# Kernel optimization log

Measured on AMD Instinct MI355X. Metric: run time of the kernel, lower is better.

Reference implementation:

```python
import jax, jax.numpy as jnp
import numpy as np

MARGIN = 0.3
EPS = 1e-12

def setup_inputs() -> dict:
    key = jax.random.key(0)
    k1, k2 = jax.random.split(key)
    n, d, num_classes = 8192, 512, 512
    inputs = jax.random.normal(k1, (n, d), dtype=jnp.float32)
    targets = jax.random.randint(k2, (n,), 0, num_classes, dtype=jnp.int64)
    return {"inputs": inputs, "targets": targets}

def reference(inputs, targets):
    n = inputs.shape[0]
    # pairwise Euclidean distances: ||xi||^2 + ||xj||^2 - 2 xi.xj, clamped & sqrt'd
    sq = jnp.sum(inputs * inputs, axis=1)  # [n]
    dist2 = sq[:, None] + sq[None, :] - 2.0 * (inputs @ inputs.T)
    dist = jnp.sqrt(jnp.clip(dist2, EPS, None))  # [n, n]
    mask = targets[:, None] == targets[None, :]  # [n, n] same-identity mask
    neg_inf = jnp.asarray(-jnp.inf, dist.dtype)
    pos_inf = jnp.asarray(jnp.inf, dist.dtype)
    dist_ap = jnp.max(jnp.where(mask, dist, neg_inf), axis=1)   # hardest positive per row
    dist_an = jnp.min(jnp.where(mask, pos_inf, dist), axis=1)   # hardest negative per row
    # MarginRankingLoss with y=1, mean reduction: mean(relu(dist_ap - dist_an + margin))
    loss = jnp.mean(jnp.maximum(dist_ap - dist_an + MARGIN, 0.0))
    return loss
```

## Files before the change

### kernel.cpp

```cpp
#include <hip/hip_runtime.h>

#define N 8192
#define D 512
#define NSB 32
#define NFULL 1024
#define NQ 64
#define NBRICKS (NFULL + NQ)
#define MARGIN 0.3f

typedef __attribute__((ext_vector_type(4))) int int4v;
typedef __attribute__((ext_vector_type(8))) int int8v;
typedef __attribute__((ext_vector_type(4))) float f32x4;

__device__ __forceinline__ void gload_lds16(const void* g, void* l) {
    __builtin_amdgcn_global_load_lds(
        (const __attribute__((address_space(1))) void*)g,
        (__attribute__((address_space(3))) void*)l,
        16, 0, 0);
}

__device__ __forceinline__ int8v load_frag8(const unsigned char* base, int row, int q) {
    const int v = (2 * q) ^ (row & 7);
    int4v lo = *(const int4v*)(base + row * 128 + v * 16);
    int4v hi = *(const int4v*)(base + row * 128 + (v ^ 1) * 16);
    return __builtin_shufflevector(lo, hi, 0, 1, 2, 3, 4, 5, 6, 7);
}

__global__ void prep_kernel(const float* __restrict__ x,
                            unsigned char* __restrict__ x8,
                            float* __restrict__ sq,
                            unsigned int* __restrict__ apU,
                            unsigned int* __restrict__ anU,
                            int* __restrict__ cnt) {
    if (blockIdx.x == 0 && threadIdx.x == 0) cnt[0] = 0;
    int w = threadIdx.x >> 6, lane = threadIdx.x & 63;
    int row = blockIdx.x * 4 + w;
    const float4* p = (const float4*)(x + (size_t)row * D) + lane * 2;
    float4 v0 = p[0], v1 = p[1];
    float s = v0.x * v0.x + v0.y * v0.y + v0.z * v0.z + v0.w * v0.w
            + v1.x * v1.x + v1.y * v1.y + v1.z * v1.z + v1.w * v1.w;
    int w0 = __builtin_amdgcn_cvt_pk_fp8_f32(v0.x, v0.y, 0, false);
    w0     = __builtin_amdgcn_cvt_pk_fp8_f32(v0.z, v0.w, w0, true);
    int w1 = __builtin_amdgcn_cvt_pk_fp8_f32(v1.x, v1.y, 0, false);
    w1     = __builtin_amdgcn_cvt_pk_fp8_f32(v1.z, v1.w, w1, true);
    ((int2*)(x8 + (size_t)row * D))[lane] = make_int2(w0, w1);
    #pragma unroll
    for (int o = 32; o > 0; o >>= 1) s += __shfl_xor(s, o);
    if (lane == 0) {
        sq[row] = s;
        apU[row] = 0u;
        anU[row] = 0x7f800000u;
    }
}

template <int TN>
__device__ __forceinline__ void brick_body(
    int rowBase, int colBase,
    const unsigned char* __restrict__ xb, const float* __restrict__ sq,
    const int* __restrict__ tgt,
    unsigned int* __restrict__ apU, unsigned int* __restrict__ anU,
    char* smem_raw, float* sqI, float* sqJ, int* tI, int* tJ) {
    constexpr int NC = TN * 32;
    unsigned char* Asm = (unsigned char*)smem_raw;
    unsigned char* Bsm = Asm + 128 * 128;
    float* redAp = (float*)smem_raw;
    float* redAn = redAp + 128 * 34;
    float* colAp = (float*)smem_raw;
    float* colAn = colAp + NC * 10;

    const int tid = threadIdx.x;
    const int w = tid >> 6, lane = tid & 63, q = lane >> 4, c = lane & 15;
    const int wm = w & 1, wn = w >> 1;

    if (tid < 128) { sqI[tid] = sq[rowBase + tid]; tI[tid] = tgt[rowBase + tid]; }
    if (tid < NC)  { sqJ[tid] = sq[colBase + tid]; tJ[tid] = tgt[colBase + tid]; }

    const unsigned char* Ag = xb + (size_t)rowBase * D;
    const unsigned char* Bg = xb + (size_t)colBase * D;

    f32x4 acc[4][TN] = {};

    for (int k0 = 0; k0 < D; k0 += 128) {
        #pragma unroll
        for (int s = 0; s < 4; s++) {
            int p = s * 256 + tid;
            int r = p >> 3, kc = (p & 7) ^ (r & 7);
            gload_lds16(Ag + (size_t)r * D + k0 + kc * 16, Asm + p * 16);
        }
        #pragma unroll
        for (int s = 0; s < TN; s++) {
            int p = s * 256 + tid;
            int r = p >> 3, kc = (p & 7) ^ (r & 7);
            gload_lds16(Bg + (size_t)r * D + k0 + kc * 16, Bsm + p * 16);
        }
        __syncthreads();
        int8v af[4];
        #pragma unroll
        for (int t = 0; t < 4; t++)
            af[t] = load_frag8(Asm, wm * 64 + t * 16 + c, q);
        constexpr int TB = (TN < 4) ? TN : 4;
        #pragma unroll
        for (int tb = 0; tb < TN; tb += TB) {
            int8v bfr[TB];
            #pragma unroll
            for (int t = 0; t < TB; t++)
                bfr[t] = load_frag8(Bsm, wn * (TN * 16) + (tb + t) * 16 + c, q);
            #pragma unroll
            for (int tm = 0; tm < 4; tm++)
                #pragma unroll
                for (int t = 0; t < TB; t++)
                    acc[tm][tb + t] = __builtin_amdgcn_mfma_scale_f32_16x16x128_f8f6f4(
                        af[tm], bfr[t], acc[tm][tb + t],
                        0, 0,
                        0, 0x7F7F7F7Fu, 0, 0x7F7F7F7Fu);
        }
        __syncthreads();
    }

    float sjc[TN]; int tjx[TN];
    #pragma unroll
    for (int tn = 0; tn < TN; tn++) {
        int col_l = wn * (TN * 16) + tn * 16 + c;
        sjc[tn] = sqJ[col_l]; tjx[tn] = tJ[col_l];
    }
    float apc[TN], anc[TN];
    #pragma unroll
    for (int tn = 0; tn < TN; tn++) { apc[tn] = -1e30f; anc[tn] = 1e30f; }
    #pragma unroll
    for (int tm = 0; tm < 4; tm++) {
        #pragma unroll
        for (int r = 0; r < 4; r++) {
            int row_l = wm * 64 + tm * 16 + q * 4 + r;
            float si = sqI[row_l]; int ti = tI[row_l];
            float rp = -1e30f, rn = 1e30f;
            #pragma unroll
            for (int tn = 0; tn < TN; tn++) {
                float p = acc[tm][tn][r];
                bool same = (ti == tjx[tn]);
                float rk = fmaf(-2.0f, p, sjc[tn]);
                float ck = fmaf(-2.0f, p, si);
                rp = fmaxf(rp, same ? rk : -1e30f);
                rn = fminf(rn, same ? 1e30f : rk);
                apc[tn] = fmaxf(apc[tn], same ? ck : -1e30f);
                anc[tn] = fminf(anc[tn], same ? 1e30f : ck);
            }
            redAp[row_l * 34 + wn * 16 + c] = rp;
            redAn[row_l * 34 + wn * 16 + c] = rn;
        }
    }
    __syncthreads();
    if (tid < 128) {
        float ap = -1e30f, an = 1e30f;
        #pragma unroll 8
        for (int u = 0; u < 32; u++) {
            ap = fmaxf(ap, redAp[tid * 34 + u]);
            an = fminf(an, redAn[tid * 34 + u]);
        }
        float apd = fmaxf(sqI[tid] + ap, 0.0f);
        float and_ = fmaxf(sqI[tid] + an, 0.0f);
        atomicMax(&apU[rowBase + tid], __float_as_uint(apd));
        atomicMin(&anU[rowBase + tid], __float_as_uint(and_));
    }
    __syncthreads();
    #pragma unroll
    for (int tn = 0; tn < TN; tn++) {
        int col_l = wn * (TN * 16) + tn * 16 + c;
        colAp[col_l * 10 + wm * 4 + q] = apc[tn];
        colAn[col_l * 10 + wm * 4 + q] = anc[tn];
    }
    __syncthreads();
    if (tid < NC) {
        float ap = -1e30f, an = 1e30f;
        #pragma unroll
        for (int u = 0; u < 8; u++) {
            ap = fmaxf(ap, colAp[tid * 10 + u]);
            an = fminf(an, colAn[tid * 10 + u]);
        }
        float apd = fmaxf(sqJ[tid] + ap, 0.0f);
        float and_ = fmaxf(sqJ[tid] + an, 0.0f);
        atomicMax(&apU[colBase + tid], __float_as_uint(apd));
        atomicMin(&anU[colBase + tid], __float_as_uint(and_));
    }
}

__global__ __launch_bounds__(256, 2)
void gemm_kernel(const unsigned char* __restrict__ xb,
                 const float* __restrict__ sq,
                 const int* __restrict__ tgt,
                 unsigned int* __restrict__ apU,
                 unsigned int* __restrict__ anU) {
    __shared__ __align__(16) char smem_raw[49152];
    __shared__ float sqI[128], sqJ[256];
    __shared__ int tI[128], tJ[256];

    const int id = blockIdx.x;
    if (id < NFULL) {
        int bj2 = (int)sqrtf((float)id + 0.5f);
        while (bj2 * bj2 > id) bj2--;
        while ((bj2 + 1) * (bj2 + 1) <= id) bj2++;
        const int bi = id - bj2 * bj2;
        brick_body<8>(bi * 128, bj2 * 256, xb, sq, tgt, apU, anU,
                      smem_raw, sqI, sqJ, tI, tJ);
    } else {
        const int h = id - NFULL;
        const int j = h >> 1, side = h & 1;
        brick_body<2>((2 * j + 1) * 128, j * 256 + 128 + side * 64,
                      xb, sq, tgt, apU, anU, smem_raw, sqI, sqJ, tI, tJ);
    }
}

__global__ void reduce_kernel(const unsigned int* __restrict__ apU,
                              const unsigned int* __restrict__ anU,
                              float* __restrict__ bsum, int* __restrict__ cnt,
                              float* __restrict__ out) {
    int tid = threadIdx.x;
    int row = blockIdx.x * 256 + tid;
    float ap = __uint_as_float(apU[row]);
    float an = __uint_as_float(anU[row]);
    float dap = sqrtf(fmaxf(ap, 1e-12f));
    float dan = sqrtf(fmaxf(an, 1e-12f));
    float v = fmaxf(dap - dan + MARGIN, 0.0f);
    #pragma unroll
    for (int o = 32; o > 0; o >>= 1) v += __shfl_xor(v, o);
    __shared__ float ss[4];
    __shared__ int amLast;
    if ((tid & 63) == 0) ss[tid >> 6] = v;
    __syncthreads();
    if (tid == 0) {
        bsum[blockIdx.x] = ss[0] + ss[1] + ss[2] + ss[3];
        __threadfence();
        amLast = (atomicAdd(cnt, 1) == N / 256 - 1);
    }
    __syncthreads();
    if (amLast && tid < 64) {
        __threadfence();
        float t = (tid < N / 256) ? bsum[tid] : 0.0f;
        #pragma unroll
        for (int o = 32; o > 0; o >>= 1) t += __shfl_xor(t, o);
        if (tid == 0) out[0] = t * (1.0f / (float)N);
    }
}

extern "C" void kernel_launch(void* const* d_in, const int* in_sizes, int n_in,
                              void* d_out, int out_size, void* d_ws, size_t ws_size,
                              hipStream_t stream) {
    const float* x  = (const float*)d_in[0];
    const int* tgt  = (const int*)d_in[1];
    float* out      = (float*)d_out;

    char* ws = (char*)d_ws;
    unsigned char* x8 = (unsigned char*)ws;
    float* sq   = (float*)(ws + (size_t)N * D);
    unsigned int* apU = (unsigned int*)(sq + N);
    unsigned int* anU = apU + N;
    float* bsum = (float*)(anU + N);
    int* cnt = (int*)(bsum + 32);

    prep_kernel<<<N / 4, 256, 0, stream>>>(x, x8, sq, apU, anU, cnt);
    gemm_kernel<<<NBRICKS, 256, 0, stream>>>(x8, sq, tgt, apU, anU);
    reduce_kernel<<<N / 256, 256, 0, stream>>>(apU, anU, bsum, cnt, out);
}
```

Before: 104.5 us.

## Switch to uniform 128x128 triangular tiles with double-buffered LDS prefetch

Replaces the 128x256 bricks plus half-bricks with uniform 128x128 tiles over the upper triangle and diagonal, with one code path. Adds two LDS buffers so the loads for the next K-step overlap the MFMA work on the current one, using explicit vmcnt waits and barriers. The goal is to hide global-to-LDS load latency and balance the work across blocks. In exchange it uses 64KB of shared memory, which may cut occupancy below the 2 blocks per CU the launch bounds ask for. Smaller tiles also mean more tiles overall, and each element of the B operand is reused less.

Result: no change. 105.6 us (+1.0%).

```diff
diff --git a/kernel.cpp b/kernel.cpp
--- a/kernel.cpp
+++ b/kernel.cpp
@@ -2,10 +2,9 @@
 
 #define N 8192
 #define D 512
-#define NSB 32
-#define NFULL 1024
-#define NQ 64
-#define NBRICKS (NFULL + NQ)
+#define NFULLP 2016
+#define NDIAG 64
+#define NBRICKS (NFULLP + NDIAG)
 #define MARGIN 0.3f
 
 typedef __attribute__((ext_vector_type(4))) int int4v;
@@ -24,6 +23,23 @@
     int4v lo = *(const int4v*)(base + row * 128 + v * 16);
     int4v hi = *(const int4v*)(base + row * 128 + (v ^ 1) * 16);
     return __builtin_shufflevector(lo, hi, 0, 1, 2, 3, 4, 5, 6, 7);
+}
+
+__device__ __forceinline__ void stage_tile(const unsigned char* Ag, unsigned char* Asm,
+                                           const unsigned char* Bg, unsigned char* Bsm,
+                                           int tid, int k0) {
+    #pragma unroll
+    for (int s = 0; s < 4; s++) {
+        int p = s * 256 + tid;
+        int r = p >> 3, kc = (p & 7) ^ (r & 7);
+        gload_lds16(Ag + (size_t)r * D + k0 + kc * 16, Asm + p * 16);
+    }
+    #pragma unroll
+    for (int s = 0; s < 4; s++) {
+        int p = s * 256 + tid;
+        int r = p >> 3, kc = (p & 7) ^ (r & 7);
+        gload_lds16(Bg + (size_t)r * D + k0 + kc * 16, Bsm + p * 16);
+    }
 }
 
 __global__ void prep_kernel(const float* __restrict__ x,
@@ -53,79 +69,78 @@
     }
 }
 
-template <int TN>
 __device__ __forceinline__ void brick_body(
     int rowBase, int colBase,
     const unsigned char* __restrict__ xb, const float* __restrict__ sq,
     const int* __restrict__ tgt,
     unsigned int* __restrict__ apU, unsigned int* __restrict__ anU,
     char* smem_raw, float* sqI, float* sqJ, int* tI, int* tJ) {
-    constexpr int NC = TN * 32;
-    unsigned char* Asm = (unsigned char*)smem_raw;
-    unsigned char* Bsm = Asm + 128 * 128;
+    unsigned char* A0 = (unsigned char*)smem_raw;
+    unsigned char* B0 = A0 + 16384;
+    unsigned char* A1 = A0 + 32768;
+    unsigned char* B1 = A0 + 49152;
     float* redAp = (float*)smem_raw;
     float* redAn = redAp + 128 * 34;
     float* colAp = (float*)smem_raw;
-    float* colAn = colAp + NC * 10;
+    float* colAn = colAp + 128 * 10;
 
     const int tid = threadIdx.x;
     const int w = tid >> 6, lane = tid & 63, q = lane >> 4, c = lane & 15;
     const int wm = w & 1, wn = w >> 1;
 
-    if (tid < 128) { sqI[tid] = sq[rowBase + tid]; tI[tid] = tgt[rowBase + tid]; }
-    if (tid < NC)  { sqJ[tid] = sq[colBase + tid]; tJ[tid] = tgt[colBase + tid]; }
+    if (tid < 128) {
+        sqI[tid] = sq[rowBase + tid]; tI[tid] = tgt[rowBase + tid];
+        sqJ[tid] = sq[colBase + tid]; tJ[tid] = tgt[colBase + tid];
+    }
 
     const unsigned char* Ag = xb + (size_t)rowBase * D;
     const unsigned char* Bg = xb + (size_t)colBase * D;
 
-    f32x4 acc[4][TN] = {};
-
-    for (int k0 = 0; k0 < D; k0 += 128) {
-        #pragma unroll
-        for (int s = 0; s < 4; s++) {
-            int p = s * 256 + tid;
-            int r = p >> 3, kc = (p & 7) ^ (r & 7);
-            gload_lds16(Ag + (size_t)r * D + k0 + kc * 16, Asm + p * 16);
-        }
-        #pragma unroll
-        for (int s = 0; s < TN; s++) {
-            int p = s * 256 + tid;
-            int r = p >> 3, kc = (p & 7) ^ (r & 7);
-            gload_lds16(Bg + (size_t)r * D + k0 + kc * 16, Bsm + p * 16);
-        }
-        __syncthreads();
-        int8v af[4];
+    f32x4 acc[4][4] = {};
+
+    stage_tile(Ag, A0, Bg, B0, tid, 0);
+    stage_tile(Ag, A1, Bg, B1, tid, 128);
+
+    #pragma unroll
+    for (int kk = 0; kk < 4; kk++) {
+        unsigned char* Asm = (kk & 1) ? A1 : A0;
+        unsigned char* Bsm = (kk & 1) ? B1 : B0;
+        if (kk == 0) asm volatile("s_waitcnt vmcnt(8)" ::: "memory");
+        else         asm volatile("s_waitcnt vmcnt(0)" ::: "memory");
+        asm volatile("s_barrier" ::: "memory");
+        __builtin_amdgcn_sched_barrier(0);
+
+        if (kk == 1) stage_tile(Ag, A0, Bg, B0, tid, 256);
+        if (kk == 2) stage_tile(Ag, A1, Bg, B1, tid, 384);
+
+        int8v af[4], bf[4];
         #pragma unroll
         for (int t = 0; t < 4; t++)
             af[t] = load_frag8(Asm, wm * 64 + t * 16 + c, q);
-        constexpr int TB = (TN < 4) ? TN : 4;
-        #pragma unroll
-        for (int tb = 0; tb < TN; tb += TB) {
-            int8v bfr[TB];
+        #pragma unroll
+        for (int t = 0; t < 4; t++)
+            bf[t] = load_frag8(Bsm, wn * 64 + t * 16 + c, q);
+
+        #pragma unroll
+        for (int tm = 0; tm < 4; tm++)
             #pragma unroll
-            for (int t = 0; t < TB; t++)
-                bfr[t] = load_frag8(Bsm, wn * (TN * 16) + (tb + t) * 16 + c, q);
-            #pragma unroll
-            for (int tm = 0; tm < 4; tm++)
-                #pragma unroll
-                for (int t = 0; t < TB; t++)
-                    acc[tm][tb + t] = __builtin_amdgcn_mfma_scale_f32_16x16x128_f8f6f4(
-                        af[tm], bfr[t], acc[tm][tb + t],
-                        0, 0,
-                        0, 0x7F7F7F7Fu, 0, 0x7F7F7F7Fu);
-        }
-        __syncthreads();
-    }
-
-    float sjc[TN]; int tjx[TN];
-    #pragma unroll
-    for (int tn = 0; tn < TN; tn++) {
-        int col_l = wn * (TN * 16) + tn * 16 + c;
+            for (int t = 0; t < 4; t++)
+                acc[tm][t] = __builtin_amdgcn_mfma_scale_f32_16x16x128_f8f6f4(
+                    af[tm], bf[t], acc[tm][t],
+                    0, 0,
+                    0, 0x7F7F7F7Fu, 0, 0x7F7F7F7Fu);
+    }
+    __syncthreads();
+
+    float sjc[4]; int tjx[4];
+    #pragma unroll
+    for (int tn = 0; tn < 4; tn++) {
+        int col_l = wn * 64 + tn * 16 + c;
         sjc[tn] = sqJ[col_l]; tjx[tn] = tJ[col_l];
     }
-    float apc[TN], anc[TN];
-    #pragma unroll
-    for (int tn = 0; tn < TN; tn++) { apc[tn] = -1e30f; anc[tn] = 1e30f; }
+    float apc[4], anc[4];
+    #pragma unroll
+    for (int tn = 0; tn < 4; tn++) { apc[tn] = -1e30f; anc[tn] = 1e30f; }
     #pragma unroll
     for (int tm = 0; tm < 4; tm++) {
         #pragma unroll
@@ -134,7 +149,7 @@
             float si = sqI[row_l]; int ti = tI[row_l];
             float rp = -1e30f, rn = 1e30f;
             #pragma unroll
-            for (int tn = 0; tn < TN; tn++) {
+            for (int tn = 0; tn < 4; tn++) {
                 float p = acc[tm][tn][r];
                 bool same = (ti == tjx[tn]);
                 float rk = fmaf(-2.0f, p, sjc[tn]);
@@ -163,13 +178,13 @@
     }
     __syncthreads();
     #pragma unroll
-    for (int tn = 0; tn < TN; tn++) {
-        int col_l = wn * (TN * 16) + tn * 16 + c;
+    for (int tn = 0; tn < 4; tn++) {
+        int col_l = wn * 64 + tn * 16 + c;
         colAp[col_l * 10 + wm * 4 + q] = apc[tn];
         colAn[col_l * 10 + wm * 4 + q] = anc[tn];
     }
     __syncthreads();
-    if (tid < NC) {
+    if (tid < 128) {
         float ap = -1e30f, an = 1e30f;
         #pragma unroll
         for (int u = 0; u < 8; u++) {
@@ -189,24 +204,22 @@
                  const int* __restrict__ tgt,
                  unsigned int* __restrict__ apU,
                  unsigned int* __restrict__ anU) {
-    __shared__ __align__(16) char smem_raw[49152];
-    __shared__ float sqI[128], sqJ[256];
-    __shared__ int tI[128], tJ[256];
+    __shared__ __align__(16) char smem_raw[65536];
+    __shared__ float sqI[128], sqJ[128];
+    __shared__ int tI[128], tJ[128];
 
     const int id = blockIdx.x;
-    if (id < NFULL) {
-        int bj2 = (int)sqrtf((float)id + 0.5f);
-        while (bj2 * bj2 > id) bj2--;
-        while ((bj2 + 1) * (bj2 + 1) <= id) bj2++;
-        const int bi = id - bj2 * bj2;
-        brick_body<8>(bi * 128, bj2 * 256, xb, sq, tgt, apU, anU,
-                      smem_raw, sqI, sqJ, tI, tJ);
+    int ri, cj;
+    if (id < NFULLP) {
+        cj = (int)((1.0f + sqrtf(1.0f + 8.0f * (float)id)) * 0.5f);
+        while (cj * (cj - 1) / 2 > id) cj--;
+        while ((cj + 1) * cj / 2 <= id) cj++;
+        ri = id - cj * (cj - 1) / 2;
     } else {
-        const int h = id - NFULL;
-        const int j = h >> 1, side = h & 1;
-        brick_body<2>((2 * j + 1) * 128, j * 256 + 128 + side * 64,
-                      xb, sq, tgt, apU, anU, smem_raw, sqI, sqJ, tI, tJ);
-    }
+        ri = cj = id - NFULLP;
+    }
+    brick_body(ri * 128, cj * 128, xb, sq, tgt, apU, anU,
+               smem_raw, sqI, sqJ, tI, tJ);
 }
 
 __global__ void reduce_kernel(const unsigned int* __restrict__ apU,
```
